# Kernel tuning notes

Measured on AMD Instinct MI355X. Metric: run time of the kernel, lower is better.

Reference implementation:

```python
import jax, jax.numpy as jnp
import numpy as np

V, D, HID = 100000, 256, 256
H = HID // 2          # per-direction LSTM hidden
K = 9                 # tagset_size - 1 (real tags + START + STOP; PAD excluded)
START, STOP = 7, 8
B, T = 128, 512


def setup_inputs() -> dict:
    key = jax.random.key(0)
    ks = jax.random.split(key, 12)
    sentence = jax.random.randint(ks[0], (B, T), 0, V, dtype=jnp.int32)
    lengths = jnp.sort(jax.random.randint(ks[1], (B,), 1, T + 1, dtype=jnp.int32))[::-1]
    lengths = lengths.at[0].set(T)  # pack_padded_sequence: descending, max == T
    s = 1.0 / np.sqrt(H)
    u = lambda k, shape: jax.random.uniform(k, shape, jnp.float32, -s, s)
    emb = jax.random.normal(ks[2], (V, D), jnp.float32)
    Wih_f, Whh_f, b_f = u(ks[3], (4 * H, D)), u(ks[4], (4 * H, H)), u(ks[5], (4 * H,))
    Wih_b, Whh_b, b_b = u(ks[6], (4 * H, D)), u(ks[7], (4 * H, H)), u(ks[8], (4 * H,))
    Wt, bt = u(ks[9], (K, HID)), u(ks[10], (K,))
    trans = jax.random.normal(ks[11], (K, K), jnp.float32)
    trans = trans.at[START, :].set(-10000.0).at[:, STOP].set(-10000.0)
    return dict(sentence=sentence, lengths=lengths, emb=emb,
                Wih_f=Wih_f, Whh_f=Whh_f, b_f=b_f,
                Wih_b=Wih_b, Whh_b=Whh_b, b_b=b_b,
                Wt=Wt, bt=bt, trans=trans)


def _bilstm_feats(sentence, lengths, emb, Wih_f, Whh_f, b_f, Wih_b, Whh_b, b_b, Wt, bt):
    x = jnp.swapaxes(emb[sentence], 0, 1)                      # [T,B,D]
    t_len, b_sz = x.shape[0], x.shape[1]
    mask = jnp.arange(t_len)[:, None] < lengths[None, :]       # [T,B], packed-seq validity

    def run(Wih, Whh, b, reverse):
        def step(carry, inp):
            h, c = carry
            xt, mt = inp
            g = xt @ Wih.T + h @ Whh.T + b                     # [B,4H], gate order i,f,g,o
            gi, gf, gg, go = jnp.split(g, 4, axis=-1)
            c_new = jax.nn.sigmoid(gf) * c + jax.nn.sigmoid(gi) * jnp.tanh(gg)
            h_new = jax.nn.sigmoid(go) * jnp.tanh(c_new)
            m = mt[:, None]
            h2 = jnp.where(m, h_new, h)                        # freeze state past length
            c2 = jnp.where(m, c_new, c)
            return (h2, c2), h2
        hdim = Whh.shape[1]
        init = (jnp.zeros((b_sz, hdim), x.dtype), jnp.zeros((b_sz, hdim), x.dtype))
        _, hs = jax.lax.scan(step, init, (x, mask), reverse=reverse)
        return hs                                              # [T,B,H]

    hf = run(Wih_f, Whh_f, b_f, False)
    hb = run(Wih_b, Whh_b, b_b, True)                          # backward starts at t=len-1 per seq
    return jnp.concatenate([hf, hb], axis=-1) @ Wt.T + bt      # [T,B,K]


def reference(sentence, lengths, emb, Wih_f, Whh_f, b_f, Wih_b, Whh_b, b_b, Wt, bt, trans):
    feats = _bilstm_feats(sentence, lengths, emb, Wih_f, Whh_f, b_f,
                          Wih_b, Whh_b, b_b, Wt, bt)           # [T,B,K]
    b_sz = feats.shape[1]
    init_fv = jnp.full((b_sz, K), -10000.0, feats.dtype).at[:, START].set(0.0)

    def vstep(fv, feat_t):
        # fv[b, prev] + trans[next, prev] -> max over prev, then add emission
        best = jnp.max(fv[:, None, :] + trans[None, :, :], axis=-1)  # [B,K]
        fv_new = best + feat_t
        return fv_new, fv_new

    _, table = jax.lax.scan(vstep, init_fv, feats)             # [T,B,K]
    final = table[lengths - 1, jnp.arange(b_sz)]               # [B,K] at each seq's last step
    terminal = final + trans[STOP]
    path_score = jnp.max(terminal, axis=1, keepdims=True)      # [B,1]
    return path_score
```

## Files before the change

### kernel.cpp

```cpp
#include <hip/hip_runtime.h>

typedef float f32x4 __attribute__((ext_vector_type(4)));
typedef _Float16 f16x8 __attribute__((ext_vector_type(8)));
typedef _Float16 f16x4 __attribute__((ext_vector_type(4)));

constexpr int kB = 128;
constexpr int kT = 512;
constexpr int kD = 256;
constexpr int kG = 512;
constexpr int kH = 128;
constexpr int kK = 9;
constexpr int kSTART = 7;
constexpr int kSTOP = 8;
constexpr int kNB = 16;


__global__ __launch_bounds__(256) void proj_kernel(
    const int* __restrict__ sentence, const int* __restrict__ lengths,
    const float* __restrict__ emb,
    const float* __restrict__ Wih_f, const float* __restrict__ b_f,
    const float* __restrict__ Wih_b, const float* __restrict__ b_b,
    _Float16* __restrict__ gi)
{
    __shared__ __align__(16) _Float16 smemA[128 * 256];
    __shared__ __align__(16) _Float16 smemW[128 * 256];

    const int g  = blockIdx.x >> 6;
    const int tc = blockIdx.x & 63;
    if (tc * 8 >= lengths[g * 16]) return;
    const int tid = threadIdx.x;

    {
        const int row = tid >> 1;
        const int kb  = (tid & 1) << 7;
        const int b   = g * 16 + (row & 15);
        const int t   = tc * 8 + (row >> 4);
        const int vocab = sentence[b * kT + t];
        const float* src = emb + (size_t)vocab * kD + kb;
        const unsigned rowbyte = row * 512;
        const unsigned sw = (row & 7) << 4;
        #pragma unroll
        for (int c = 0; c < 16; ++c) {
            float4 x0 = *(const float4*)(src + c * 8);
            float4 x1 = *(const float4*)(src + c * 8 + 4);
            f16x8 pk;
            pk[0] = (_Float16)x0.x; pk[1] = (_Float16)x0.y;
            pk[2] = (_Float16)x0.z; pk[3] = (_Float16)x0.w;
            pk[4] = (_Float16)x1.x; pk[5] = (_Float16)x1.y;
            pk[6] = (_Float16)x1.z; pk[7] = (_Float16)x1.w;
            unsigned byteoff = rowbyte + ((unsigned)((kb + c * 8) * 2) ^ sw);
            *(f16x8*)((char*)smemA + byteoff) = pk;
        }
    }

    const int w    = tid >> 6;
    const int lane = tid & 63;
    const int wr = w >> 1, wc = w & 1;
    const int l15 = lane & 15, l4 = lane >> 4;

    int lene[4];
    #pragma unroll
    for (int rg = 0; rg < 4; ++rg)
        lene[rg] = lengths[g * 16 + l4 * 4 + rg];

    for (int by = 0; by < 8; ++by) {
        const int dir = by >> 2;
        const int q   = by & 3;
        __syncthreads();
        {
            const int row = tid >> 1;
            const int kb  = (tid & 1) << 7;
            const float* src = (dir == 0 ? Wih_f : Wih_b)
                               + (size_t)(q * 128 + row) * kD + kb;
            const unsigned rowbyte = row * 512;
            const unsigned sw = (row & 7) << 4;
            #pragma unroll
            for (int c = 0; c < 16; ++c) {
                float4 x0 = *(const float4*)(src + c * 8);
                float4 x1 = *(const float4*)(src + c * 8 + 4);
                f16x8 pk;
                pk[0] = (_Float16)x0.x; pk[1] = (_Float16)x0.y;
                pk[2] = (_Float16)x0.z; pk[3] = (_Float16)x0.w;
                pk[4] = (_Float16)x1.x; pk[5] = (_Float16)x1.y;
                pk[6] = (_Float16)x1.z; pk[7] = (_Float16)x1.w;
                unsigned byteoff = rowbyte + ((unsigned)((kb + c * 8) * 2) ^ sw);
                *(f16x8*)((char*)smemW + byteoff) = pk;
            }
        }
        __syncthreads();

        f32x4 zero = {0.f, 0.f, 0.f, 0.f};
        f32x4 acc[4][4];
        #pragma unroll
        for (int mf = 0; mf < 4; ++mf)
            #pragma unroll
            for (int nf = 0; nf < 4; ++nf) acc[mf][nf] = zero;

        #pragma unroll
        for (int kk = 0; kk < 8; ++kk) {
            f16x8 afr[4], bfr[4];
            #pragma unroll
            for (int mf = 0; mf < 4; ++mf) {
                int row = wr * 64 + mf * 16 + l15;
                unsigned byteoff = row * 512 +
                    ((unsigned)(kk * 64 + l4 * 16) ^ (unsigned)((row & 7) << 4));
                afr[mf] = *(const f16x8*)((const char*)smemA + byteoff);
            }
            #pragma unroll
            for (int nf = 0; nf < 4; ++nf) {
                int row = wc * 64 + nf * 16 + l15;
                unsigned byteoff = row * 512 +
                    ((unsigned)(kk * 64 + l4 * 16) ^ (unsigned)((row & 7) << 4));
                bfr[nf] = *(const f16x8*)((const char*)smemW + byteoff);
            }
            #pragma unroll
            for (int mf = 0; mf < 4; ++mf)
                #pragma unroll
                for (int nf = 0; nf < 4; ++nf)
                    acc[mf][nf] = __builtin_amdgcn_mfma_f32_16x16x32_f16(
                        afr[mf], bfr[nf], acc[mf][nf], 0, 0, 0);
        }

        const float* biasp = (dir == 0) ? b_f : b_b;
        _Float16* dbase = gi + (size_t)(dir * 8 + g) * kT * 8192;
        #pragma unroll
        for (int nf = 0; nf < 4; ++nf) {
            int u = wc * 64 + nf * 16 + l15;
            float bias = biasp[q * 128 + u];
            #pragma unroll
            for (int mf = 0; mf < 4; ++mf) {
                int t = tc * 8 + wr * 4 + mf;
                f16x4 pk;
                #pragma unroll
                for (int rg = 0; rg < 4; ++rg) {
                    float v = (t < lene[rg]) ? (acc[mf][nf][rg] + bias) : 0.f;
                    pk[rg] = (_Float16)v;
                }
                *(f16x4*)(dbase + (size_t)t * 8192 + (q * 128 + u) * 16 + l4 * 4) = pk;
            }
        }
    }
}

__device__ inline void wg_barrier() {
    asm volatile("s_waitcnt lgkmcnt(0)" ::: "memory");
    __builtin_amdgcn_s_barrier();
    asm volatile("" ::: "memory");
}

#define LOADSET(GP, SS)                                                       \
    do {                                                                      \
        int tt = dir ? (smax - 1 - (SS)) : (SS);                              \
        const _Float16* rp = glane + (ptrdiff_t)tt * 8192;                    \
        GP##0 = *(const f16x4*)(rp);                                          \
        GP##1 = *(const f16x4*)(rp + 2048);                                   \
        GP##2 = *(const f16x4*)(rp + 4096);                                   \
        GP##3 = *(const f16x4*)(rp + 6144);                                   \
    } while (0)

#define ACTIVATE(reg, ACC0, ACC1, ACC2, ACC3, HPK)                            \
    do {                                                                      \
        float i_ = ACC0, f_ = ACC1, g_ = ACC2, o_ = ACC3;                     \
        float Ei = __expf(-i_), Ef = __expf(-f_);                             \
        float Eg = __expf(-2.f * g_), Eo = __expf(-o_);                       \
        float a1 = 1.f + Ei, a2 = 1.f + Eg, a3 = 1.f + Ef;                    \
        float a12 = a1 * a2;                                                  \
        float num = cst[reg] * a12 + (1.f - Eg) * a3;                         \
        float cn = num * __builtin_amdgcn_rcpf(a3 * a12);                     \
        cst[reg] = cn;                                                        \
        float cc = fminf(fmaxf(cn, -15.f), 15.f);                             \
        float Ec = __expf(-2.f * cc);                                         \
        float hn = (1.f - Ec) *                                               \
            __builtin_amdgcn_rcpf((1.f + Eo) * (1.f + Ec));                   \
        HPK[reg] = (_Float16)hn;                                              \
    } while (0)

#define LSTM_BODY(PH, GP)                                                     \
    do {                                                                      \
        const int tb = dir ? (smax - 1 - (s + PH)) : (s + PH);                \
        f32x4 acc[4];                                                         \
        _Pragma("unroll")                                                     \
        for (int reg = 0; reg < 4; ++reg) {                                   \
            acc[0][reg] = (float)GP##0[reg];                                  \
            acc[1][reg] = (float)GP##1[reg];                                  \
            acc[2][reg] = (float)GP##2[reg];                                  \
            acc[3][reg] = (float)GP##3[reg];                                  \
        }                                                                     \
        LOADSET(GP, s + PH + 4);                                              \
        _Pragma("unroll")                                                     \
        for (int kk = 0; kk < 4; ++kk)                                        \
            _Pragma("unroll")                                                 \
            for (int q = 0; q < 4; ++q)                                       \
                acc[q] = __builtin_amdgcn_mfma_f32_16x16x32_f16(              \
                    afr[kk], bfr[q][kk], acc[q], 0, 0, 0);                    \
        f16x4 hpk;                                                            \
        _Pragma("unroll")                                                     \
        for (int reg = 0; reg < 4; ++reg) {                                   \
            ACTIVATE(reg, acc[0][reg], acc[1][reg], acc[2][reg],              \
                     acc[3][reg], hpk);                                       \
            int rr = l4 * 4 + reg;                                            \
            unsigned bo = ((unsigned)(rr * 256 + u * 2)) ^                    \
                          (unsigned)((rr & 7) << 4);                          \
            *(_Float16*)((char*)hbuf[(PH) & 1] + bo) = hpk[reg];              \
        }                                                                     \
        if ((unsigned)tb < (unsigned)smax) {    \
            *(f16x4*)(hrow_base + (size_t)tb * 8192) = hpk;                   \
        }                                                                     \
        wg_barrier();                                                         \
        {                                                                     \
            const unsigned sw2 = (unsigned)((l15 & 7) << 4);                  \
            _Pragma("unroll")                                                 \
            for (int kk = 0; kk < 4; ++kk) {                                  \
                unsigned bo = ((unsigned)(l15 * 256 + kk * 64 + l4 * 16)) ^   \
                              sw2;                                            \
                afr[kk] = *(const f16x8*)((const char*)hbuf[(PH) & 1] + bo);  \
            }                                                                 \
        }                                                                     \
    } while (0)

__global__ __launch_bounds__(512) void lstm_kernel(
    const _Float16* gi, _Float16* hws, const int* __restrict__ lengths,
    const float* __restrict__ Whh_f, const float* __restrict__ Whh_b)
{
    const int bid = blockIdx.x;
    const int dir = bid >> 3;
    const int g   = bid & 7;
    const int tid = threadIdx.x;
    const int w   = tid >> 6;
    const int l   = tid & 63;
    const int l15 = l & 15, l4 = l >> 4;

    __shared__ __align__(16) _Float16 hbuf[2][kNB * kH];

    const float* Whh = dir ? Whh_b : Whh_f;
    f16x8 bfr[4][4];
    #pragma unroll
    for (int q = 0; q < 4; ++q) {
        #pragma unroll
        for (int kk = 0; kk < 4; ++kk) {
            int n  = q * 128 + w * 16 + l15;
            int k0 = kk * 32 + l4 * 8;
            const float* src = Whh + (size_t)n * kH + k0;
            float4 x0 = *(const float4*)(src);
            float4 x1 = *(const float4*)(src + 4);
            f16x8 v;
            v[0] = (_Float16)x0.x; v[1] = (_Float16)x0.y;
            v[2] = (_Float16)x0.z; v[3] = (_Float16)x0.w;
            v[4] = (_Float16)x1.x; v[5] = (_Float16)x1.y;
            v[6] = (_Float16)x1.z; v[7] = (_Float16)x1.w;
            bfr[q][kk] = v;
        }
    }

    const int smax = lengths[g * kNB];
    const int smax_pad = (smax + 3) & ~3;

    const int u = w * 16 + l15;
    float cst[4] = {0.f, 0.f, 0.f, 0.f};
    f16x8 afr[4];
    #pragma unroll
    for (int kk = 0; kk < 4; ++kk)
        #pragma unroll
        for (int j = 0; j < 8; ++j) afr[kk][j] = (_Float16)0.f;

    const _Float16* glane = gi + (size_t)(dir * 8 + g) * kT * 8192
                               + (size_t)(u * 16 + l4 * 4);
    _Float16* hrow_base = hws + (size_t)(dir * 8 + g) * kT * 8192
                              + (size_t)tid * 4;

    f16x4 gA0, gA1, gA2, gA3, gB0, gB1, gB2, gB3;
    f16x4 gC0, gC1, gC2, gC3, gD0, gD1, gD2, gD3;
    LOADSET(gA, 0); LOADSET(gB, 1); LOADSET(gC, 2); LOADSET(gD, 3);

    for (int s = 0; s < smax_pad; s += 4) {
        LSTM_BODY(0, gA);
        LSTM_BODY(1, gB);
        LSTM_BODY(2, gC);
        LSTM_BODY(3, gD);
    }
}

__global__ __launch_bounds__(256) void feats_kernel(
    const _Float16* __restrict__ hws, const float* __restrict__ Wt,
    const float* __restrict__ bt, float* __restrict__ fsum)
{
    __shared__ _Float16 hf[2048], hb[2048];
    __shared__ float wts[kK * 256];
    __shared__ float bts[kK];
    const int g = blockIdx.x >> 9;
    const int t = blockIdx.x & 511;
    const int tid = threadIdx.x;

    *(f16x8*)&hf[tid * 8] =
        *(const f16x8*)(hws + ((size_t)g * kT + t) * 8192 + tid * 8);
    *(f16x8*)&hb[tid * 8] =
        *(const f16x8*)(hws + ((size_t)(8 + g) * kT + t) * 8192 + tid * 8);
    for (int i = tid; i < kK * 256; i += 256) wts[i] = Wt[i];
    if (tid < kK) bts[tid] = bt[tid];
    __syncthreads();

    if (tid < 144) {
        const int k = tid >> 4;
        const int r = tid & 15;
        float acc = bts[k];
        #pragma unroll 8
        for (int uu = 0; uu < kH; ++uu) {
            int idx = (uu >> 4) * 256 + (r >> 2) * 64 + (uu & 15) * 4 + (r & 3);
            acc += (float)hf[idx] * wts[k * 256 + uu] +
                   (float)hb[idx] * wts[k * 256 + 128 + uu];
        }
        fsum[((size_t)(g * 16 + r) * kT + t) * kK + k] = acc;
    }
}

__global__ __launch_bounds__(512) void viterbi_kernel(
    const int* __restrict__ lengths, const float* __restrict__ trans,
    const float* __restrict__ fsumg, float* __restrict__ out)
{
    constexpr float NEG = -1e30f;
    constexpr int RA = 0;
    constexpr int RB = 128 * 81;
    const int b = blockIdx.x;
    const int len = lengths[b];
    const int tid = threadIdx.x;

    __shared__ float tree[(128 + 64) * 81];
    __shared__ float fsum[kT * kK];
    __shared__ float trs[81];
    __shared__ float red[16];

    if (tid < 81) trs[tid] = trans[tid];
    for (int idx = tid; idx < len * kK; idx += 512)
        fsum[idx] = fsumg[(size_t)b * kT * kK + idx];
    __syncthreads();

    for (int task = tid; task < 128 * 9; task += 512) {
        int s = task / 9, j = task - s * 9;
        int tb = 4 * s;
        float uu[9];
        #pragma unroll
        for (int m = 0; m < 9; ++m)
            uu[m] = (tb < len) ? (trs[m * 9 + j] + fsum[tb * 9 + m])
                               : ((m == j) ? 0.f : NEG);
        #pragma unroll
        for (int q = 1; q < 4; ++q) {
            int t = tb + q;
            if (t < len) {
                float un[9];
                #pragma unroll
                for (int k = 0; k < 9; ++k) {
                    float v = trs[k * 9] + uu[0];
                    #pragma unroll
                    for (int m = 1; m < 9; ++m)
                        v = fmaxf(v, trs[k * 9 + m] + uu[m]);
                    un[k] = v + fsum[t * 9 + k];
                }
                #pragma unroll
                for (int k = 0; k < 9; ++k) uu[k] = un[k];
            }
        }
        #pragma unroll
        for (int k = 0; k < 9; ++k)
            tree[RA + s * 81 + k * 9 + j] = uu[k];
    }
    __syncthreads();

    int soff = RA, doff = RB;
    for (int np = 64; np >= 1; np >>= 1) {
        for (int idx = tid; idx < np * 81; idx += 512) {
            int s = idx / 81, o = idx - s * 81;
            int k = o / 9, j = o - k * 9;
            const float* A  = tree + soff + (2 * s + 1) * 81;
            const float* Bm = tree + soff + (2 * s) * 81;
            float v = A[k * 9] + Bm[j];
            #pragma unroll
            for (int m = 1; m < 9; ++m)
                v = fmaxf(v, A[k * 9 + m] + Bm[m * 9 + j]);
            tree[doff + s * 81 + o] = v;
        }
        int tmp = soff; soff = doff; doff = tmp;
        __syncthreads();
    }
    if (tid < kK) {
        int k = tid;
        float fv = tree[soff + k * 9 + kSTART];
        #pragma unroll
        for (int j = 0; j < 9; ++j)
            if (j != kSTART) fv = fmaxf(fv, tree[soff + k * 9 + j] - 10000.f);
        red[k] = fv + trs[kSTOP * 9 + k];
    }
    __syncthreads();
    if (tid == 0) {
        float m = red[0];
        #pragma unroll
        for (int k = 1; k < 9; ++k) m = fmaxf(m, red[k]);
        out[b] = m;
    }
}

extern "C" void kernel_launch(void* const* d_in, const int* in_sizes, int n_in,
                              void* d_out, int out_size, void* d_ws, size_t ws_size,
                              hipStream_t stream) {
    const int*   sentence = (const int*)d_in[0];
    const int*   lengths  = (const int*)d_in[1];
    const float* emb      = (const float*)d_in[2];
    const float* Wih_f    = (const float*)d_in[3];
    const float* Whh_f    = (const float*)d_in[4];
    const float* b_f      = (const float*)d_in[5];
    const float* Wih_b    = (const float*)d_in[6];
    const float* Whh_b    = (const float*)d_in[7];
    const float* b_b      = (const float*)d_in[8];
    const float* Wt       = (const float*)d_in[9];
    const float* bt       = (const float*)d_in[10];
    const float* trans    = (const float*)d_in[11];
    float* out = (float*)d_out;

    char* ws = (char*)d_ws;
    const size_t gi_bytes = (size_t)2 * kB * kT * kG * sizeof(_Float16);
    _Float16* gi   = (_Float16*)ws;
    _Float16* hws  = (_Float16*)ws;
    float*    fsum = (float*)(ws + gi_bytes);

    proj_kernel<<<512, 256, 0, stream>>>(sentence, lengths, emb,
                                         Wih_f, b_f, Wih_b, b_b, gi);
    lstm_kernel<<<16, 512, 0, stream>>>(gi, hws, lengths, Whh_f, Whh_b);
    feats_kernel<<<4096, 256, 0, stream>>>(hws, Wt, bt, fsum);
    viterbi_kernel<<<128, 512, 0, stream>>>(lengths, trans, fsum, out);
}
```

Measured before the change: 616.5 us.

## Interleave forward and backward LSTM directions in one workgroup per batch group

```diff
diff --git a/kernel.cpp b/kernel.cpp
--- a/kernel.cpp
+++ b/kernel.cpp
@@ -148,26 +148,25 @@
     asm volatile("" ::: "memory");
 }
 
-#define LOADSET(GP, SS)                                                       \
+#define LOADSET(GP, BASE, TT)                                                 \
     do {                                                                      \
-        int tt = dir ? (smax - 1 - (SS)) : (SS);                              \
-        const _Float16* rp = glane + (ptrdiff_t)tt * 8192;                    \
+        const _Float16* rp = (BASE) + (ptrdiff_t)(TT) * 8192;                 \
         GP##0 = *(const f16x4*)(rp);                                          \
         GP##1 = *(const f16x4*)(rp + 2048);                                   \
         GP##2 = *(const f16x4*)(rp + 4096);                                   \
         GP##3 = *(const f16x4*)(rp + 6144);                                   \
     } while (0)
 
-#define ACTIVATE(reg, ACC0, ACC1, ACC2, ACC3, HPK)                            \
+#define ACTIVATE(CST, reg, ACC0, ACC1, ACC2, ACC3, HPK)                       \
     do {                                                                      \
         float i_ = ACC0, f_ = ACC1, g_ = ACC2, o_ = ACC3;                     \
         float Ei = __expf(-i_), Ef = __expf(-f_);                             \
         float Eg = __expf(-2.f * g_), Eo = __expf(-o_);                       \
         float a1 = 1.f + Ei, a2 = 1.f + Eg, a3 = 1.f + Ef;                    \
         float a12 = a1 * a2;                                                  \
-        float num = cst[reg] * a12 + (1.f - Eg) * a3;                         \
+        float num = CST[reg] * a12 + (1.f - Eg) * a3;                         \
         float cn = num * __builtin_amdgcn_rcpf(a3 * a12);                     \
-        cst[reg] = cn;                                                        \
+        CST[reg] = cn;                                                        \
         float cc = fminf(fmaxf(cn, -15.f), 15.f);                             \
         float Ec = __expf(-2.f * cc);                                         \
         float hn = (1.f - Ec) *                                               \
@@ -175,9 +174,18 @@
         HPK[reg] = (_Float16)hn;                                              \
     } while (0)
 
-#define LSTM_BODY(PH, GP)                                                     \
+#define HALF_STEP(PH, GP, BASE, TT, TTPF, BFR, CST, HB, HROW, TGUARD)         \
     do {                                                                      \
-        const int tb = dir ? (smax - 1 - (s + PH)) : (s + PH);                \
+        f16x8 afr[4];                                                         \
+        {                                                                     \
+            const unsigned sw2 = (unsigned)((l15 & 7) << 4);                  \
+            _Pragma("unroll")                                                 \
+            for (int kk = 0; kk < 4; ++kk) {                                  \
+                unsigned bo = ((unsigned)(l15 * 256 + kk * 64 + l4 * 16)) ^   \
+                              sw2;                                            \
+                afr[kk] = *(const f16x8*)((const char*)HB[(PH) ^ 1] + bo);    \
+            }                                                                 \
+        }                                                                     \
         f32x4 acc[4];                                                         \
         _Pragma("unroll")                                                     \
         for (int reg = 0; reg < 4; ++reg) {                                   \
@@ -186,97 +194,110 @@
             acc[2][reg] = (float)GP##2[reg];                                  \
             acc[3][reg] = (float)GP##3[reg];                                  \
         }                                                                     \
-        LOADSET(GP, s + PH + 4);                                              \
+        LOADSET(GP, BASE, TTPF);                                              \
         _Pragma("unroll")                                                     \
         for (int kk = 0; kk < 4; ++kk)                                        \
             _Pragma("unroll")                                                 \
             for (int q = 0; q < 4; ++q)                                       \
                 acc[q] = __builtin_amdgcn_mfma_f32_16x16x32_f16(              \
-                    afr[kk], bfr[q][kk], acc[q], 0, 0, 0);                    \
+                    afr[kk], BFR[q][kk], acc[q], 0, 0, 0);                    \
         f16x4 hpk;                                                            \
         _Pragma("unroll")                                                     \
         for (int reg = 0; reg < 4; ++reg) {                                   \
-            ACTIVATE(reg, acc[0][reg], acc[1][reg], acc[2][reg],              \
+            ACTIVATE(CST, reg, acc[0][reg], acc[1][reg], acc[2][reg],         \
                      acc[3][reg], hpk);                                       \
             int rr = l4 * 4 + reg;                                            \
             unsigned bo = ((unsigned)(rr * 256 + u * 2)) ^                    \
                           (unsigned)((rr & 7) << 4);                          \
-            *(_Float16*)((char*)hbuf[(PH) & 1] + bo) = hpk[reg];              \
+            *(_Float16*)((char*)HB[PH] + bo) = hpk[reg];                      \
         }                                                                     \
-        if ((unsigned)tb < (unsigned)smax) {    \
-            *(f16x4*)(hrow_base + (size_t)tb * 8192) = hpk;                   \
+        if (TGUARD) {                           \
+            *(f16x4*)(HROW + (ptrdiff_t)(TT) * 8192) = hpk;                   \
         }                                                                     \
+    } while (0)
+
+#define SUPERSTEP(PH, GF, GB)                                                 \
+    do {                                                                      \
+        const int tF = s + (PH);                                              \
+        const int tB = smax - 1 - (s + (PH));                                 \
+        HALF_STEP(PH, GF, glaneF, tF, tF + 2, bfrF, cstF, hbufF, hrowF,       \
+                  (tF < smax));                                               \
+        HALF_STEP(PH, GB, glaneB, tB, tB - 2, bfrB, cstB, hbufB, hrowB,       \
+                  (tB >= 0));                                                 \
         wg_barrier();                                                         \
-        {                                                                     \
-            const unsigned sw2 = (unsigned)((l15 & 7) << 4);                  \
-            _Pragma("unroll")                                                 \
-            for (int kk = 0; kk < 4; ++kk) {                                  \
-                unsigned bo = ((unsigned)(l15 * 256 + kk * 64 + l4 * 16)) ^   \
-                              sw2;                                            \
-                afr[kk] = *(const f16x8*)((const char*)hbuf[(PH) & 1] + bo);  \
-            }                                                                 \
-        }                                                                     \
     } while (0)
 
 __global__ __launch_bounds__(512) void lstm_kernel(
     const _Float16* gi, _Float16* hws, const int* __restrict__ lengths,
     const float* __restrict__ Whh_f, const float* __restrict__ Whh_b)
 {
-    const int bid = blockIdx.x;
-    const int dir = bid >> 3;
-    const int g   = bid & 7;
+    const int g   = blockIdx.x;
     const int tid = threadIdx.x;
     const int w   = tid >> 6;
     const int l   = tid & 63;
     const int l15 = l & 15, l4 = l >> 4;
 
-    __shared__ __align__(16) _Float16 hbuf[2][kNB * kH];
-
-    const float* Whh = dir ? Whh_b : Whh_f;
-    f16x8 bfr[4][4];
+    __shared__ __align__(16) _Float16 hbufF[2][kNB * kH];
+    __shared__ __align__(16) _Float16 hbufB[2][kNB * kH];
+
+    f16x8 bfrF[4][4], bfrB[4][4];
     #pragma unroll
     for (int q = 0; q < 4; ++q) {
         #pragma unroll
         for (int kk = 0; kk < 4; ++kk) {
             int n  = q * 128 + w * 16 + l15;
             int k0 = kk * 32 + l4 * 8;
-            const float* src = Whh + (size_t)n * kH + k0;
-            float4 x0 = *(const float4*)(src);
-            float4 x1 = *(const float4*)(src + 4);
-            f16x8 v;
-            v[0] = (_Float16)x0.x; v[1] = (_Float16)x0.y;
-            v[2] = (_Float16)x0.z; v[3] = (_Float16)x0.w;
-            v[4] = (_Float16)x1.x; v[5] = (_Float16)x1.y;
-            v[6] = (_Float16)x1.z; v[7] = (_Float16)x1.w;
-            bfr[q][kk] = v;
+            const float* srcF = Whh_f + (size_t)n * kH + k0;
+            const float* srcB = Whh_b + (size_t)n * kH + k0;
+            float4 xf0 = *(const float4*)(srcF);
+            float4 xf1 = *(const float4*)(srcF + 4);
+            float4 xb0 = *(const float4*)(srcB);
+            float4 xb1 = *(const float4*)(srcB + 4);
+            f16x8 vf, vb;
+            vf[0] = (_Float16)xf0.x; vf[1] = (_Float16)xf0.y;
+            vf[2] = (_Float16)xf0.z; vf[3] = (_Float16)xf0.w;
+            vf[4] = (_Float16)xf1.x; vf[5] = (_Float16)xf1.y;
+            vf[6] = (_Float16)xf1.z; vf[7] = (_Float16)xf1.w;
+            vb[0] = (_Float16)xb0.x; vb[1] = (_Float16)xb0.y;
+            vb[2] = (_Float16)xb0.z; vb[3] = (_Float16)xb0.w;
+            vb[4] = (_Float16)xb1.x; vb[5] = (_Float16)xb1.y;
+            vb[6] = (_Float16)xb1.z; vb[7] = (_Float16)xb1.w;
+            bfrF[q][kk] = vf;
+            bfrB[q][kk] = vb;
         }
     }
 
     const int smax = lengths[g * kNB];
-    const int smax_pad = (smax + 3) & ~3;
+    const int smax_pad = (smax + 1) & ~1;
 
     const int u = w * 16 + l15;
-    float cst[4] = {0.f, 0.f, 0.f, 0.f};
-    f16x8 afr[4];
-    #pragma unroll
-    for (int kk = 0; kk < 4; ++kk)
-        #pragma unroll
-        for (int j = 0; j < 8; ++j) afr[kk][j] = (_Float16)0.f;
-
-    const _Float16* glane = gi + (size_t)(dir * 8 + g) * kT * 8192
-                               + (size_t)(u * 16 + l4 * 4);
-    _Float16* hrow_base = hws + (size_t)(dir * 8 + g) * kT * 8192
-                              + (size_t)tid * 4;
-
-    f16x4 gA0, gA1, gA2, gA3, gB0, gB1, gB2, gB3;
-    f16x4 gC0, gC1, gC2, gC3, gD0, gD1, gD2, gD3;
-    LOADSET(gA, 0); LOADSET(gB, 1); LOADSET(gC, 2); LOADSET(gD, 3);
-
-    for (int s = 0; s < smax_pad; s += 4) {
-        LSTM_BODY(0, gA);
-        LSTM_BODY(1, gB);
-        LSTM_BODY(2, gC);
-        LSTM_BODY(3, gD);
+    float cstF[4] = {0.f, 0.f, 0.f, 0.f};
+    float cstB[4] = {0.f, 0.f, 0.f, 0.f};
+
+    const _Float16* glaneF = gi + (size_t)g * kT * 8192
+                                + (size_t)(u * 16 + l4 * 4);
+    const _Float16* glaneB = gi + (size_t)(8 + g) * kT * 8192
+                                + (size_t)(u * 16 + l4 * 4);
+    _Float16* hrowF = hws + (size_t)g * kT * 8192 + (size_t)tid * 4;
+    _Float16* hrowB = hws + (size_t)(8 + g) * kT * 8192 + (size_t)tid * 4;
+
+    for (int i = tid; i < kNB * kH; i += 512) {
+        hbufF[1][i] = (_Float16)0.f;
+        hbufB[1][i] = (_Float16)0.f;
+    }
+
+    f16x4 gF00, gF01, gF02, gF03, gF10, gF11, gF12, gF13;
+    f16x4 gB00, gB01, gB02, gB03, gB10, gB11, gB12, gB13;
+    LOADSET(gF0, glaneF, 0);
+    LOADSET(gF1, glaneF, 1);
+    LOADSET(gB0, glaneB, smax - 1);
+    LOADSET(gB1, glaneB, smax - 2);
+
+    wg_barrier();
+
+    for (int s = 0; s < smax_pad; s += 2) {
+        SUPERSTEP(0, gF0, gB0);
+        SUPERSTEP(1, gF1, gB1);
     }
 }
 
@@ -423,7 +444,7 @@
 
     proj_kernel<<<512, 256, 0, stream>>>(sentence, lengths, emb,
                                          Wih_f, b_f, Wih_b, b_b, gi);
-    lstm_kernel<<<16, 512, 0, stream>>>(gi, hws, lengths, Whh_f, Whh_b);
+    lstm_kernel<<<8, 512, 0, stream>>>(gi, hws, lengths, Whh_f, Whh_b);
     feats_kernel<<<4096, 256, 0, stream>>>(hws, Wt, bt, fsum);
     viterbi_kernel<<<128, 512, 0, stream>>>(lengths, trans, fsum, out);
 }
```

Measured after the change: 1.033 ms. 1.68x slower.

## Load input-projection weights directly from global into MFMA fragments; batch feats timesteps

Applied to the files above, without the earlier changes.

```diff
diff --git a/kernel.cpp b/kernel.cpp
--- a/kernel.cpp
+++ b/kernel.cpp
@@ -23,7 +23,6 @@
     _Float16* __restrict__ gi)
 {
     __shared__ __align__(16) _Float16 smemA[128 * 256];
-    __shared__ __align__(16) _Float16 smemW[128 * 256];
 
     const int g  = blockIdx.x >> 6;
     const int tc = blockIdx.x & 63;
@@ -63,31 +62,12 @@
     for (int rg = 0; rg < 4; ++rg)
         lene[rg] = lengths[g * 16 + l4 * 4 + rg];
 
+    __syncthreads();
+
     for (int by = 0; by < 8; ++by) {
         const int dir = by >> 2;
         const int q   = by & 3;
-        __syncthreads();
-        {
-            const int row = tid >> 1;
-            const int kb  = (tid & 1) << 7;
-            const float* src = (dir == 0 ? Wih_f : Wih_b)
-                               + (size_t)(q * 128 + row) * kD + kb;
-            const unsigned rowbyte = row * 512;
-            const unsigned sw = (row & 7) << 4;
-            #pragma unroll
-            for (int c = 0; c < 16; ++c) {
-                float4 x0 = *(const float4*)(src + c * 8);
-                float4 x1 = *(const float4*)(src + c * 8 + 4);
-                f16x8 pk;
-                pk[0] = (_Float16)x0.x; pk[1] = (_Float16)x0.y;
-                pk[2] = (_Float16)x0.z; pk[3] = (_Float16)x0.w;
-                pk[4] = (_Float16)x1.x; pk[5] = (_Float16)x1.y;
-                pk[6] = (_Float16)x1.z; pk[7] = (_Float16)x1.w;
-                unsigned byteoff = rowbyte + ((unsigned)((kb + c * 8) * 2) ^ sw);
-                *(f16x8*)((char*)smemW + byteoff) = pk;
-            }
-        }
-        __syncthreads();
+        const float* Wp = (dir == 0) ? Wih_f : Wih_b;
 
         f32x4 zero = {0.f, 0.f, 0.f, 0.f};
         f32x4 acc[4][4];
@@ -108,10 +88,16 @@
             }
             #pragma unroll
             for (int nf = 0; nf < 4; ++nf) {
-                int row = wc * 64 + nf * 16 + l15;
-                unsigned byteoff = row * 512 +
-                    ((unsigned)(kk * 64 + l4 * 16) ^ (unsigned)((row & 7) << 4));
-                bfr[nf] = *(const f16x8*)((const char*)smemW + byteoff);
+                int n = q * 128 + wc * 64 + nf * 16 + l15;
+                const float* src = Wp + (size_t)n * kD + kk * 32 + l4 * 8;
+                float4 x0 = *(const float4*)(src);
+                float4 x1 = *(const float4*)(src + 4);
+                f16x8 v;
+                v[0] = (_Float16)x0.x; v[1] = (_Float16)x0.y;
+                v[2] = (_Float16)x0.z; v[3] = (_Float16)x0.w;
+                v[4] = (_Float16)x1.x; v[5] = (_Float16)x1.y;
+                v[6] = (_Float16)x1.z; v[7] = (_Float16)x1.w;
+                bfr[nf] = v;
             }
             #pragma unroll
             for (int mf = 0; mf < 4; ++mf)
@@ -284,32 +270,37 @@
     const _Float16* __restrict__ hws, const float* __restrict__ Wt,
     const float* __restrict__ bt, float* __restrict__ fsum)
 {
-    __shared__ _Float16 hf[2048], hb[2048];
+    __shared__ _Float16 hf[4][2048], hb[4][2048];
     __shared__ float wts[kK * 256];
     __shared__ float bts[kK];
-    const int g = blockIdx.x >> 9;
-    const int t = blockIdx.x & 511;
+    const int g  = blockIdx.x >> 7;
+    const int t0 = (blockIdx.x & 127) * 4;
     const int tid = threadIdx.x;
 
-    *(f16x8*)&hf[tid * 8] =
-        *(const f16x8*)(hws + ((size_t)g * kT + t) * 8192 + tid * 8);
-    *(f16x8*)&hb[tid * 8] =
-        *(const f16x8*)(hws + ((size_t)(8 + g) * kT + t) * 8192 + tid * 8);
+    #pragma unroll
+    for (int j = 0; j < 4; ++j) {
+        *(f16x8*)&hf[j][tid * 8] =
+            *(const f16x8*)(hws + ((size_t)g * kT + t0 + j) * 8192 + tid * 8);
+        *(f16x8*)&hb[j][tid * 8] =
+            *(const f16x8*)(hws + ((size_t)(8 + g) * kT + t0 + j) * 8192 + tid * 8);
+    }
     for (int i = tid; i < kK * 256; i += 256) wts[i] = Wt[i];
     if (tid < kK) bts[tid] = bt[tid];
     __syncthreads();
 
-    if (tid < 144) {
-        const int k = tid >> 4;
-        const int r = tid & 15;
+    for (int task = tid; task < 4 * 144; task += 256) {
+        const int tl  = task / 144;
+        const int rem = task - tl * 144;
+        const int k = rem >> 4;
+        const int r = rem & 15;
         float acc = bts[k];
         #pragma unroll 8
         for (int uu = 0; uu < kH; ++uu) {
             int idx = (uu >> 4) * 256 + (r >> 2) * 64 + (uu & 15) * 4 + (r & 3);
-            acc += (float)hf[idx] * wts[k * 256 + uu] +
-                   (float)hb[idx] * wts[k * 256 + 128 + uu];
-        }
-        fsum[((size_t)(g * 16 + r) * kT + t) * kK + k] = acc;
+            acc += (float)hf[tl][idx] * wts[k * 256 + uu] +
+                   (float)hb[tl][idx] * wts[k * 256 + 128 + uu];
+        }
+        fsum[((size_t)(g * 16 + r) * kT + t0 + tl) * kK + k] = acc;
     }
 }
 
@@ -424,6 +415,6 @@
     proj_kernel<<<512, 256, 0, stream>>>(sentence, lengths, emb,
                                          Wih_f, b_f, Wih_b, b_b, gi);
     lstm_kernel<<<16, 512, 0, stream>>>(gi, hws, lengths, Whh_f, Whh_b);
-    feats_kernel<<<4096, 256, 0, stream>>>(hws, Wt, bt, fsum);
+    feats_kernel<<<1024, 256, 0, stream>>>(hws, Wt, bt, fsum);
     viterbi_kernel<<<128, 512, 0, stream>>>(lengths, trans, fsum, out);
 }
```

After: 710.8 us. 1.15x slower.
